# Optimization experiments

Hardware: AMD Instinct MI355X
Metric: run time of the kernel (lower is better)

Reference implementation:

```python
import jax, jax.numpy as jnp
import numpy as np

# dims
B, C, H, W = 32, 512, 32, 32
E, A, NC, DC, R, K = 256, 32, 8, 32, 24, 3
PW = NC * DC  # 256


def _ln(x, g, b, eps=1e-5):
    m = jnp.mean(x, axis=-1, keepdims=True)
    v = jnp.mean(jnp.square(x - m), axis=-1, keepdims=True)
    return (x - m) / jnp.sqrt(v + eps) * g + b


def setup_inputs() -> dict:
    key = jax.random.key(0)
    ks = jax.random.split(key, 12)
    s = 0.05
    f32 = jnp.float32
    return {
        "x": jax.random.normal(ks[0], (B, C, H, W), f32),
        "geo_state": jax.random.normal(ks[1], (B, PW), f32) * s,
        "W_svd": jax.random.normal(ks[2], (R, PW), f32) * s,
        "b_svd": jnp.zeros((PW,), f32),
        "g_svd": jnp.ones((PW,), f32),
        "beta_svd": jnp.zeros((PW,), f32),
        "W_emb": jax.random.normal(ks[3], (C, E), f32) * s,
        "g_emb": jnp.ones((E,), f32),
        "beta_emb": jnp.zeros((E,), f32),
        "anchors": jax.random.normal(ks[4], (A, E), f32),
        "Wc1": jax.random.normal(ks[5], (NC, A, 2 * DC), f32) * s,
        "bc1": jnp.zeros((NC, 2 * DC), f32),
        "Wc2": jax.random.normal(ks[6], (NC, 2 * DC, DC), f32) * s,
        "bc2": jnp.zeros((NC, DC), f32),
        "g_c": jnp.ones((NC, DC), f32),
        "beta_c": jnp.zeros((NC, DC), f32),
        "W_mod": jax.random.normal(ks[7], (3 * PW, C), f32) * s,
        "b_mod": jnp.zeros((C,), f32),
        "geo_gate": jnp.full((PW,), -3.0, f32),
        "W_geo": jax.random.normal(ks[8], (PW, PW), f32) * s,
        "b_geo": jnp.zeros((PW,), f32),
        "g_geo": jnp.ones((PW,), f32),
        "beta_geo": jnp.zeros((PW,), f32),
    }


def reference(x, geo_state, W_svd, b_svd, g_svd, beta_svd, W_emb, g_emb,
              beta_emb, anchors, Wc1, bc1, Wc2, bc2, g_c, beta_c, W_mod,
              b_mod, geo_gate, W_geo, b_geo, g_geo, beta_geo):
    Bx, Cx, Hx, Wx = x.shape
    HWx = Hx * Wx
    # --- SVD observer: top-R singular values via channel Gram eigvals ---
    X = x.reshape(Bx, Cx, HWx)
    Gm = jnp.einsum('bcn,bdn->bcd', X, X) / HWx           # (B, C, C)
    ev = jnp.linalg.eigvalsh(Gm)                           # ascending
    S = jnp.sqrt(jnp.clip(ev[:, ::-1][:, :R], 0.0))        # (B, R)
    svd_raw = jnp.log1p(S)
    svd_ctx = jax.nn.gelu(_ln(svd_raw @ W_svd + b_svd, g_svd, beta_svd),
                          approximate=False)               # (B, PW)
    # --- embedding: 1x1 conv + global avg pool (commute) + LN + L2 norm ---
    emb = jnp.einsum('bchw,ce->be', x, W_emb) / HWx        # (B, E)
    emb = _ln(emb, g_emb, beta_emb)
    emb = emb / jnp.maximum(jnp.linalg.norm(emb, axis=-1, keepdims=True), 1e-12)
    # --- anchor cosine geometry (anchors detached) ---
    an = anchors / jnp.maximum(jnp.linalg.norm(anchors, axis=-1, keepdims=True), 1e-12)
    an = jax.lax.stop_gradient(an)
    cos = emb @ an.T                                       # (B, A)
    tri = 1.0 - cos
    # --- cm_gate: softmax over n_neighbors nearest anchors ---
    topv, topi = jax.lax.top_k(cos, K)
    wgt = jax.nn.softmax(topv, axis=-1)                    # (B, K)
    oneh = jax.nn.one_hot(topi, A, dtype=x.dtype)          # (B, K, A)
    gate_values = jnp.einsum('bk,bka->ba', wgt, oneh)      # (B, A)
    tri_gated = tri * gate_values
    # --- grouped compartment MLPs (the Python loop, batched) ---
    h = jax.nn.gelu(jnp.einsum('ba,cad->bcd', tri_gated, Wc1) + bc1,
                    approximate=False)                     # (B, NC, 2*DC)
    pc = jnp.einsum('bcd,cde->bce', h, Wc2) + bc2          # (B, NC, DC)
    pc = _ln(pc, g_c, beta_c)
    pw = pc.reshape(Bx, PW)
    # --- channel modulation ---
    mod_in = jnp.concatenate([pw, svd_ctx, geo_state], axis=-1)
    cw = jax.nn.sigmoid(mod_in @ W_mod + b_mod)            # (B, C)
    x_out = x * cw[:, :, None, None]
    # --- gated residual geo-state update ---
    g = jax.nn.sigmoid(geo_gate)
    geo_out = geo_state + g * _ln(pw @ W_geo + b_geo, g_geo, beta_geo)
    return (x_out, geo_out)
```

## Files before the change

kernel.cpp:

```cpp
#include <hip/hip_runtime.h>
#include <hip/hip_bf16.h>

typedef unsigned short u16;
typedef unsigned int u32;
typedef __attribute__((ext_vector_type(8))) short short8;
typedef __attribute__((ext_vector_type(4))) float f32x4;

#define NB 32
#define NC_ 512
#define HW 1024
#define NE 256
#define NA 32
#define NR 24
#define PW_ 256
#define MLAN 128
#define NV 56

__device__ inline float b2f(u16 u) { return __uint_as_float(((u32)u) << 16); }
__device__ inline u16 f2b(float f) {
    u32 x = __float_as_uint(f);
    u32 r = x + 0x7FFFu + ((x >> 16) & 1u);
    return (u16)(r >> 16);
}
__device__ inline float gelu_exact(float x) {
    return 0.5f * x * (1.0f + erff(x * 0.70710678118654752f));
}
__device__ inline float sigmoidf_(float x) { return 1.0f / (1.0f + expf(-x)); }

template <int NW>
__device__ inline float block_reduce_sum(float x, volatile float* red) {
#pragma unroll
    for (int m = 32; m >= 1; m >>= 1) x += __shfl_xor(x, m);
    const int lane = threadIdx.x & 63, wid = threadIdx.x >> 6;
    __syncthreads();
    if (lane == 0) red[wid] = x;
    __syncthreads();
    float s = 0.f;
#pragma unroll
    for (int i = 0; i < NW; i++) s += red[i];
    return s;
}

__global__ __launch_bounds__(256) void gram_kernel(const float* __restrict__ x,
                                                   u16* __restrict__ Gp) {
    __shared__ __align__(16) u16 Ai[128][72];
    __shared__ __align__(16) u16 Bj[128][72];
    const int b = blockIdx.y;
    const int i0 = (blockIdx.x >> 2) * 128;
    const int j0 = (blockIdx.x & 3) * 128;
    const int t = threadIdx.x;
    const int lane = t & 63, wid = t >> 6;
    const int wm = (wid >> 1) * 64, wn = (wid & 1) * 64;
    f32x4 acc[4][4] = {};
    const float* xb = x + (size_t)b * NC_ * HW;

    for (int kc = 0; kc < HW; kc += 64) {
#pragma unroll
        for (int i = 0; i < 8; i++) {
            int idx = t + 256 * i;
            int r = idx >> 4, c4 = (idx & 15) * 4;
            float4 qa = *(const float4*)(xb + (size_t)(i0 + r) * HW + kc + c4);
            float4 qb = *(const float4*)(xb + (size_t)(j0 + r) * HW + kc + c4);
            Ai[r][c4 + 0] = f2b(qa.x); Ai[r][c4 + 1] = f2b(qa.y);
            Ai[r][c4 + 2] = f2b(qa.z); Ai[r][c4 + 3] = f2b(qa.w);
            Bj[r][c4 + 0] = f2b(qb.x); Bj[r][c4 + 1] = f2b(qb.y);
            Bj[r][c4 + 2] = f2b(qb.z); Bj[r][c4 + 3] = f2b(qb.w);
        }
        __syncthreads();
#pragma unroll
        for (int ks = 0; ks < 64; ks += 32) {
            const int kk = ks + (lane >> 4) * 8;
            short8 af[4], bf[4];
#pragma unroll
            for (int m = 0; m < 4; m++) af[m] = *(const short8*)&Ai[wm + m * 16 + (lane & 15)][kk];
#pragma unroll
            for (int n = 0; n < 4; n++) bf[n] = *(const short8*)&Bj[wn + n * 16 + (lane & 15)][kk];
#pragma unroll
            for (int m = 0; m < 4; m++)
#pragma unroll
                for (int n = 0; n < 4; n++)
                    acc[m][n] = __builtin_amdgcn_mfma_f32_16x16x32_bf16(af[m], bf[n], acc[m][n], 0, 0, 0);
        }
        __syncthreads();
    }
    const float scale = 1.0f / 1024.0f;
    u16* Gb = Gp + (size_t)b * NC_ * NC_;
#pragma unroll
    for (int m = 0; m < 4; m++) {
#pragma unroll
        for (int n = 0; n < 4; n++) {
            int row = i0 + wm + m * 16 + (lane >> 4) * 4;
            int col = j0 + wn + n * 16 + (lane & 15);
#pragma unroll
            for (int r = 0; r < 4; r++)
                Gb[(size_t)(row + r) * NC_ + col] = f2b(acc[m][n][r] * scale);
        }
    }
}

__global__ __launch_bounds__(256) void colsum_kernel(const float* __restrict__ x,
                                                     float* __restrict__ cs) {
    const int row = blockIdx.x * 4 + (threadIdx.x >> 6);
    const int lane = threadIdx.x & 63;
    const float* p = x + (size_t)row * HW;
    float s = 0.f;
    for (int i = lane; i < HW; i += 64) s += p[i];
#pragma unroll
    for (int m = 32; m >= 1; m >>= 1) s += __shfl_xor(s, m);
    if (lane == 0) cs[row] = s;
}

__global__ __launch_bounds__(1024, 4) void lanczos_kernel(const u16* __restrict__ Gp,
                                                          float* __restrict__ V,
                                                          float* __restrict__ svd_raw) {
    __shared__ __align__(16) float Vl[NV][512];
    __shared__ __align__(16) float v[512], w[512];
    __shared__ float v2[528];
    __shared__ float wpart[16][8][68];
    __shared__ float sub2[2][512];
    __shared__ float red[16], red2[16];
    __shared__ float al[MLAN], be[MLAN + 1], cc[MLAN];
    const int b = blockIdx.x;
    const int t = threadIdx.x;
    const int lane = t & 63, wid = t >> 6;
    const int el = t & 511, half = t >> 9;
    const int e8 = el & 7, l8 = el >> 3;
    const u16* Gb = Gp + (size_t)b * NC_ * NC_;
    const u16* gp = Gb + (size_t)(wid * 32) * NC_ + lane * 8;
    float* Vb = V + (size_t)b * MLAN * 512;

    u32 h = (u32)el * 2654435761u ^ ((u32)b * 0x9E3779B9u);
    h ^= h >> 16; h *= 0x85EBCA6Bu; h ^= h >> 13; h *= 0xC2B2AE35u; h ^= h >> 16;
    float vt = (float)(h & 0xFFFFFFu) * (1.0f / 16777216.0f) - 0.5f;
    float nrm = block_reduce_sum<16>(half == 0 ? vt * vt : 0.f, red);
    vt *= rsqrtf(nrm);
    if (half == 0) {
        v[el] = vt;
        v2[e8 * 66 + l8] = vt;
        Vl[0][el] = vt;
    }
    float vprev = 0.f, beta = 0.f;
    __syncthreads();

    for (int j = 0; j < MLAN; j++) {
        float a0 = 0.f, a1 = 0.f, a2 = 0.f, a3 = 0.f;
        float a4 = 0.f, a5 = 0.f, a6 = 0.f, a7 = 0.f;
        const float* vk = v + wid * 32;
#pragma unroll 16
        for (int kk = 0; kk < 32; kk++) {
            short8 g = *(const short8*)(gp + (size_t)kk * NC_);
            float vv = vk[kk];
            a0 += b2f((u16)g[0]) * vv;
            a1 += b2f((u16)g[1]) * vv;
            a2 += b2f((u16)g[2]) * vv;
            a3 += b2f((u16)g[3]) * vv;
            a4 += b2f((u16)g[4]) * vv;
            a5 += b2f((u16)g[5]) * vv;
            a6 += b2f((u16)g[6]) * vv;
            a7 += b2f((u16)g[7]) * vv;
        }
        wpart[wid][0][lane] = a0; wpart[wid][1][lane] = a1;
        wpart[wid][2][lane] = a2; wpart[wid][3][lane] = a3;
        wpart[wid][4][lane] = a4; wpart[wid][5][lane] = a5;
        wpart[wid][6][lane] = a6; wpart[wid][7][lane] = a7;
        float ap = a0 * v2[lane] + a1 * v2[66 + lane]
                 + a2 * v2[132 + lane] + a3 * v2[198 + lane]
                 + a4 * v2[264 + lane] + a5 * v2[330 + lane]
                 + a6 * v2[396 + lane] + a7 * v2[462 + lane];
#pragma unroll
        for (int m = 32; m >= 1; m >>= 1) ap += __shfl_xor(ap, m);
        if (lane == 0) red[wid] = ap;
        __syncthreads();

        float acc = 0.f;
#pragma unroll
        for (int p = 0; p < 16; p++) acc += wpart[p][e8][l8];
        float alpha = 0.f;
#pragma unroll
        for (int i = 0; i < 16; i++) alpha += red[i];
        float wt = acc - alpha * vt - beta * vprev;
        if (half == 0) w[el] = wt;
        float pz = wt * wt;
#pragma unroll
        for (int m = 32; m >= 1; m >>= 1) pz += __shfl_xor(pz, m);
        if (lane == 0 && wid < 8) red2[wid] = pz;
        __syncthreads();
        float nb0 = 0.f;
#pragma unroll
        for (int i = 0; i < 8; i++) nb0 += red2[i];
        const float gscale = nb0 + alpha * alpha + beta * beta;

        float nb = 0.f;
        for (int pass = 0;; pass++) {
            const float4 wv0 = *(const float4*)&w[lane * 4];
            const float4 wv1 = *(const float4*)&w[256 + lane * 4];
            for (int i = wid; i <= j; i += 16) {
                float4 x0, x1;
                if (i < NV) {
                    x0 = *(const float4*)&Vl[i][lane * 4];
                    x1 = *(const float4*)&Vl[i][256 + lane * 4];
                } else {
                    const float* Vi = Vb + (size_t)i * 512;
                    x0 = *(const float4*)(Vi + lane * 4);
                    x1 = *(const float4*)(Vi + 256 + lane * 4);
                }
                float p = x0.x * wv0.x + x0.y * wv0.y + x0.z * wv0.z + x0.w * wv0.w
                        + x1.x * wv1.x + x1.y * wv1.y + x1.z * wv1.z + x1.w * wv1.w;
#pragma unroll
                for (int m = 32; m >= 1; m >>= 1) p += __shfl_xor(p, m);
                if (lane == 0) cc[i] = p;
            }
            __syncthreads();
            const int n = j + 1, ns = n >> 1;
            const int ib = half ? ns : 0, ie = half ? n : ns;
            float sub = 0.f;
            int i = ib;
            const int iLe = (ie < NV) ? ie : NV;
            for (; i + 4 <= iLe; i += 4)
                sub += cc[i + 0] * Vl[i + 0][el] + cc[i + 1] * Vl[i + 1][el]
                     + cc[i + 2] * Vl[i + 2][el] + cc[i + 3] * Vl[i + 3][el];
            for (; i < iLe; i++) sub += cc[i] * Vl[i][el];
            if (i < ib) i = ib;
            for (; i + 4 <= ie; i += 4)
                sub += cc[i + 0] * Vb[(size_t)(i + 0) * 512 + el]
                     + cc[i + 1] * Vb[(size_t)(i + 1) * 512 + el]
                     + cc[i + 2] * Vb[(size_t)(i + 2) * 512 + el]
                     + cc[i + 3] * Vb[(size_t)(i + 3) * 512 + el];
            for (; i < ie; i++) sub += cc[i] * Vb[(size_t)i * 512 + el];
            sub2[half][el] = sub;
            __syncthreads();
            wt = wt - sub2[0][el] - sub2[1][el];
            if (half == 0) w[el] = wt;
            float pn = wt * wt;
#pragma unroll
            for (int m = 32; m >= 1; m >>= 1) pn += __shfl_xor(pn, m);
            if (lane == 0 && wid < 8) red[wid] = pn;
            __syncthreads();
            nb = 0.f;
#pragma unroll
            for (int q = 0; q < 8; q++) nb += red[q];
            if (pass == 1 || (nb > 0.5f * nb0 && nb0 > 1e-8f * gscale)) break;
            nb0 = nb;
        }
        float betn = sqrtf(nb);
        bool ok = (betn > 1e-20f) && (betn == betn) && !isinf(betn);
        if (t == 0) { al[j] = alpha; be[j + 1] = ok ? betn : 0.f; }
        float inv = ok ? 1.0f / betn : 0.f;
        vprev = vt;
        vt = ok ? wt * inv : 0.f;
        if (half == 0) {
            v[el] = vt;
            v2[e8 * 66 + l8] = vt;
            if (j + 1 < NV) Vl[j + 1][el] = vt;
            else if (j + 1 < MLAN) Vb[(size_t)(j + 1) * 512 + el] = vt;
        }
        beta = ok ? betn : 0.f;
        __syncthreads();
    }

    if (t < NR) {
        float lo = 1e30f, hi = -1e30f;
        for (int i = 0; i < MLAN; i++) {
            float bl = (i > 0) ? fabsf(be[i]) : 0.f;
            float br = (i + 1 < MLAN) ? fabsf(be[i + 1]) : 0.f;
            lo = fminf(lo, al[i] - bl - br);
            hi = fmaxf(hi, al[i] + bl + br);
        }
        const int i0 = MLAN - 1 - t;
        for (int it = 0; it < 30; it++) {
            float mid = 0.5f * (lo + hi);
            int cnt = 0;
            float d = 1.0f;
            for (int i = 0; i < MLAN; i++) {
                float bb2 = (i > 0) ? be[i] * be[i] : 0.f;
                float dp = d;
                if (fabsf(dp) < 1e-30f) dp = (dp < 0.f) ? -1e-30f : 1e-30f;
                d = (al[i] - mid) - bb2 / dp;
                cnt += (d < 0.f);
            }
            if (cnt > i0) hi = mid; else lo = mid;
        }
        float ev = fmaxf(0.5f * (lo + hi), 0.f);
        float val = log1pf(sqrtf(ev));
        if (!(val == val) || isinf(val)) val = 1.0f;
        svd_raw[b * NR + t] = val;
    }
}

__global__ __launch_bounds__(256) void embgate_kernel(
    const float* __restrict__ cs, const float* __restrict__ W_emb,
    const float* __restrict__ g_emb, const float* __restrict__ beta_emb,
    const float* __restrict__ anchors, float* __restrict__ tg_out) {
    const int b = blockIdx.x, t = threadIdx.x;
    __shared__ float csl[512], embv[256], cosv[32], tgs[32];
    __shared__ float red[4];

    for (int i = t; i < 512; i += 256) csl[i] = cs[b * 512 + i];
    __syncthreads();

    float e = 0.f;
    for (int c = 0; c < 512; c++) e += csl[c] * W_emb[c * NE + t];
    e *= (1.0f / 1024.0f);
    float mean = block_reduce_sum<4>(e, red) * (1.0f / 256.0f);
    float dv = e - mean;
    float var = block_reduce_sum<4>(dv * dv, red) * (1.0f / 256.0f);
    e = dv * rsqrtf(var + 1e-5f) * g_emb[t] + beta_emb[t];
    float nn = block_reduce_sum<4>(e * e, red);
    e = e / fmaxf(sqrtf(nn), 1e-12f);
    embv[t] = e;
    __syncthreads();

    if (t < 32) {
        float p = 0.f, na = 0.f;
        for (int q = 0; q < 256; q++) {
            float av = anchors[t * NE + q];
            p += embv[q] * av;
            na += av * av;
        }
        cosv[t] = p / fmaxf(sqrtf(na), 1e-12f);
    }
    __syncthreads();

    if (t == 0) {
        int i1 = 0, i2 = 0, i3 = 0;
        float v1 = -1e30f, v2 = -1e30f, v3 = -1e30f;
        for (int a = 0; a < 32; a++) {
            float cv = cosv[a];
            if (cv > v1) { v3 = v2; i3 = i2; v2 = v1; i2 = i1; v1 = cv; i1 = a; }
            else if (cv > v2) { v3 = v2; i3 = i2; v2 = cv; i2 = a; }
            else if (cv > v3) { v3 = cv; i3 = a; }
        }
        float e2 = expf(v2 - v1), e3 = expf(v3 - v1);
        float ss = 1.0f + e2 + e3;
        for (int a = 0; a < 32; a++) tgs[a] = 0.f;
        tgs[i1] = (1.0f - v1) * 1.0f / ss;
        tgs[i2] = (1.0f - v2) * e2 / ss;
        tgs[i3] = (1.0f - v3) * e3 / ss;
    }
    __syncthreads();
    if (t < 32) tg_out[b * 32 + t] = tgs[t];
}

__global__ __launch_bounds__(256) void mlp_kernel(
    const float* __restrict__ tg, const float* __restrict__ Wc1,
    const float* __restrict__ bc1, const float* __restrict__ Wc2,
    const float* __restrict__ bc2, const float* __restrict__ g_c,
    const float* __restrict__ beta_c, float* __restrict__ pw_out) {
    const int b = blockIdx.x, t = threadIdx.x;
    __shared__ float tgl[32], hbuf[512], pcb[256];

    if (t < 32) tgl[t] = tg[b * 32 + t];
    __syncthreads();

    for (int o = t; o < 512; o += 256) {
        int c = o >> 6, d = o & 63;
        float s = bc1[c * 64 + d];
        for (int a = 0; a < 32; a++) s += tgl[a] * Wc1[(c * 32 + a) * 64 + d];
        hbuf[o] = gelu_exact(s);
    }
    __syncthreads();

    const int c = t >> 5, e = t & 31;
    float s = bc2[c * 32 + e];
    for (int d = 0; d < 64; d++) s += hbuf[c * 64 + d] * Wc2[(c * 64 + d) * 32 + e];
    pcb[t] = s;
    __syncthreads();

    float mean = 0.f;
    for (int k = 0; k < 32; k++) mean += pcb[c * 32 + k];
    mean *= (1.0f / 32.0f);
    float var = 0.f;
    for (int k = 0; k < 32; k++) { float dd = pcb[c * 32 + k] - mean; var += dd * dd; }
    var *= (1.0f / 32.0f);
    pw_out[b * PW_ + t] = (s - mean) * rsqrtf(var + 1e-5f) * g_c[c * 32 + e] + beta_c[c * 32 + e];
}

__global__ __launch_bounds__(256) void ctx_kernel(
    const float* __restrict__ svd_raw, const float* __restrict__ W_svd,
    const float* __restrict__ b_svd, const float* __restrict__ g_svd,
    const float* __restrict__ beta_svd, float* __restrict__ ctx_out) {
    const int b = blockIdx.x, t = threadIdx.x;
    __shared__ float rawv[NR];
    __shared__ float red[4];
    if (t < NR) rawv[t] = svd_raw[b * NR + t];
    __syncthreads();
    float sv = b_svd[t];
    for (int r = 0; r < NR; r++) sv += rawv[r] * W_svd[r * PW_ + t];
    float mean = block_reduce_sum<4>(sv, red) * (1.0f / 256.0f);
    float dv = sv - mean;
    float var = block_reduce_sum<4>(dv * dv, red) * (1.0f / 256.0f);
    ctx_out[b * PW_ + t] = gelu_exact(dv * rsqrtf(var + 1e-5f) * g_svd[t] + beta_svd[t]);
}

__global__ __launch_bounds__(256) void cwgeo_kernel(
    const float* __restrict__ pw, const float* __restrict__ ctx,
    const float* __restrict__ geo_state, const float* __restrict__ W_mod,
    const float* __restrict__ b_mod, const float* __restrict__ geo_gate,
    const float* __restrict__ W_geo, const float* __restrict__ b_geo,
    const float* __restrict__ g_geo, const float* __restrict__ beta_geo,
    float* __restrict__ cw, float* __restrict__ out_geo) {
    const int b = blockIdx.x, t = threadIdx.x;
    __shared__ float mi[768];
    __shared__ float red[4];
    mi[t] = pw[b * PW_ + t];
    mi[256 + t] = ctx[b * PW_ + t];
    float geo = geo_state[b * PW_ + t];
    mi[512 + t] = geo;
    __syncthreads();

    float gg = b_geo[t];
    for (int q = 0; q < PW_; q++) gg += mi[q] * W_geo[q * PW_ + t];
    float gmean = block_reduce_sum<4>(gg, red) * (1.0f / 256.0f);
    float gdv = gg - gmean;
    float gvar = block_reduce_sum<4>(gdv * gdv, red) * (1.0f / 256.0f);
    float lnv = gdv * rsqrtf(gvar + 1e-5f) * g_geo[t] + beta_geo[t];
    out_geo[b * PW_ + t] = geo + sigmoidf_(geo_gate[t]) * lnv;

    for (int c = t; c < 512; c += 256) {
        float s = b_mod[c];
        for (int k = 0; k < 768; k++) s += mi[k] * W_mod[k * NC_ + c];
        cw[b * NC_ + c] = sigmoidf_(s);
    }
}

__global__ __launch_bounds__(256) void modulate_kernel(const float* __restrict__ x,
                                                       const float* __restrict__ cw,
                                                       float* __restrict__ out) {
    const int i4 = blockIdx.x * 256 + threadIdx.x;
    const float4* xp = (const float4*)x;
    float4 q = xp[i4];
    const float wv = cw[i4 >> 8];
    float4 o;
    o.x = q.x * wv; o.y = q.y * wv; o.z = q.z * wv; o.w = q.w * wv;
    ((float4*)out)[i4] = o;
}

extern "C" void kernel_launch(void* const* d_in, const int* in_sizes, int n_in,
                              void* d_out, int out_size, void* d_ws, size_t ws_size,
                              hipStream_t stream) {
    const float* x = (const float*)d_in[0];
    const float* geo_state = (const float*)d_in[1];
    const float* W_svd = (const float*)d_in[2];
    const float* b_svd = (const float*)d_in[3];
    const float* g_svd = (const float*)d_in[4];
    const float* beta_svd = (const float*)d_in[5];
    const float* W_emb = (const float*)d_in[6];
    const float* g_emb = (const float*)d_in[7];
    const float* beta_emb = (const float*)d_in[8];
    const float* anchors = (const float*)d_in[9];
    const float* Wc1 = (const float*)d_in[10];
    const float* bc1 = (const float*)d_in[11];
    const float* Wc2 = (const float*)d_in[12];
    const float* bc2 = (const float*)d_in[13];
    const float* g_c = (const float*)d_in[14];
    const float* beta_c = (const float*)d_in[15];
    const float* W_mod = (const float*)d_in[16];
    const float* b_mod = (const float*)d_in[17];
    const float* geo_gate = (const float*)d_in[18];
    const float* W_geo = (const float*)d_in[19];
    const float* b_geo = (const float*)d_in[20];
    const float* g_geo = (const float*)d_in[21];
    const float* beta_geo = (const float*)d_in[22];

    char* ob = (char*)d_out;
    u16* G = (u16*)(ob);
    float* V = (float*)(ob + 16777216);
    float* cs = (float*)(ob + 25165824);
    float* svdraw = (float*)(ob + 25231360);
    float* tg = (float*)(ob + 25234432);
    float* pw = (float*)(ob + 25238528);
    float* ctxb = (float*)(ob + 25271296);
    float* cw = (float*)d_ws;

    float* outx = (float*)d_out;
    float* outg = outx + 16777216;

    gram_kernel<<<dim3(16, 32), dim3(256), 0, stream>>>(x, G);
    colsum_kernel<<<dim3(4096), dim3(256), 0, stream>>>(x, cs);
    lanczos_kernel<<<dim3(32), dim3(1024), 0, stream>>>(G, V, svdraw);
    embgate_kernel<<<dim3(32), dim3(256), 0, stream>>>(cs, W_emb, g_emb, beta_emb, anchors, tg);
    mlp_kernel<<<dim3(32), dim3(256), 0, stream>>>(tg, Wc1, bc1, Wc2, bc2, g_c, beta_c, pw);
    ctx_kernel<<<dim3(32), dim3(256), 0, stream>>>(svdraw, W_svd, b_svd, g_svd, beta_svd, ctxb);
    cwgeo_kernel<<<dim3(32), dim3(256), 0, stream>>>(pw, ctxb, geo_state, W_mod, b_mod,
                                                     geo_gate, W_geo, b_geo, g_geo, beta_geo,
                                                     cw, outg);
    modulate_kernel<<<dim3(16384), dim3(256), 0, stream>>>(x, cw, outx);
}
```

Measured before the change: 1.847 ms.

## Store unnormalized Lanczos vectors, fuse reorthogonalization subtraction, cache Gram rows in registers

The Lanczos loop now keeps unnormalized residual vectors and applies the 1/beta scaling lazily through per-vector scale factors (sc2_, invc). That removes the separate normalize-and-store step and the barrier at the end of each iteration. Reorthogonalization projection and subtraction are fused: each wave accumulates its p*V contributions in registers and writes them to a shared scratch buffer. This replaces the cc array and the second half-split subtraction pass with its extra barrier. The first 12 rows of each wave's bf16 Gram slice are preloaded into registers, which raises register pressure at 1024 threads per block and may change numerical stability slightly.

After: 2.011 ms. 1.09x slower.

```diff
diff --git a/kernel.cpp b/kernel.cpp
--- a/kernel.cpp
+++ b/kernel.cpp
@@ -15,6 +15,7 @@
 #define PW_ 256
 #define MLAN 128
 #define NV 56
+#define NCACHE 12
 
 __device__ inline float b2f(u16 u) { return __uint_as_float(((u32)u) << 16); }
 __device__ inline u16 f2b(float f) {
@@ -114,12 +115,11 @@
                                                           float* __restrict__ V,
                                                           float* __restrict__ svd_raw) {
     __shared__ __align__(16) float Vl[NV][512];
-    __shared__ __align__(16) float v[512], w[512];
+    __shared__ __align__(16) float w[512];
     __shared__ float v2[528];
-    __shared__ float wpart[16][8][68];
-    __shared__ float sub2[2][512];
-    __shared__ float red[16], red2[16];
-    __shared__ float al[MLAN], be[MLAN + 1], cc[MLAN];
+    __shared__ __align__(16) float scr[16][544];
+    __shared__ float red[16], red2[8], red3[8];
+    __shared__ float al[MLAN], be[MLAN + 1], sc2_[MLAN + 1];
     const int b = blockIdx.x;
     const int t = threadIdx.x;
     const int lane = t & 63, wid = t >> 6;
@@ -129,25 +129,35 @@
     const u16* gp = Gb + (size_t)(wid * 32) * NC_ + lane * 8;
     float* Vb = V + (size_t)b * MLAN * 512;
 
+    u32 gc[NCACHE * 4];
+#pragma unroll
+    for (int kk = 0; kk < NCACHE; kk++) {
+        short8 g = *(const short8*)(gp + (size_t)kk * NC_);
+        const u32* gu = (const u32*)&g;
+        gc[kk * 4 + 0] = gu[0]; gc[kk * 4 + 1] = gu[1];
+        gc[kk * 4 + 2] = gu[2]; gc[kk * 4 + 3] = gu[3];
+    }
+
     u32 h = (u32)el * 2654435761u ^ ((u32)b * 0x9E3779B9u);
     h ^= h >> 16; h *= 0x85EBCA6Bu; h ^= h >> 13; h *= 0xC2B2AE35u; h ^= h >> 16;
-    float vt = (float)(h & 0xFFFFFFu) * (1.0f / 16777216.0f) - 0.5f;
-    float nrm = block_reduce_sum<16>(half == 0 ? vt * vt : 0.f, red);
-    vt *= rsqrtf(nrm);
+    float vt0 = (float)(h & 0xFFFFFFu) * (1.0f / 16777216.0f) - 0.5f;
+    float nrm = block_reduce_sum<16>(half == 0 ? vt0 * vt0 : 0.f, red);
+    vt0 *= rsqrtf(nrm);
     if (half == 0) {
-        v[el] = vt;
-        v2[e8 * 66 + l8] = vt;
-        Vl[0][el] = vt;
-    }
-    float vprev = 0.f, beta = 0.f;
+        w[el] = vt0;
+        v2[e8 * 66 + l8] = vt0;
+        Vl[0][el] = vt0;
+    }
+    if (t == 0) sc2_[0] = 1.0f;
+    float rw = vt0, invc = 1.0f, rwp = 0.f, invp = 0.f, beta = 0.f;
     __syncthreads();
 
     for (int j = 0; j < MLAN; j++) {
         float a0 = 0.f, a1 = 0.f, a2 = 0.f, a3 = 0.f;
         float a4 = 0.f, a5 = 0.f, a6 = 0.f, a7 = 0.f;
-        const float* vk = v + wid * 32;
-#pragma unroll 16
-        for (int kk = 0; kk < 32; kk++) {
+        const float* vk = w + wid * 32;
+#pragma unroll 5
+        for (int kk = NCACHE; kk < 32; kk++) {
             short8 g = *(const short8*)(gp + (size_t)kk * NC_);
             float vv = vk[kk];
             a0 += b2f((u16)g[0]) * vv;
@@ -159,10 +169,24 @@
             a6 += b2f((u16)g[6]) * vv;
             a7 += b2f((u16)g[7]) * vv;
         }
-        wpart[wid][0][lane] = a0; wpart[wid][1][lane] = a1;
-        wpart[wid][2][lane] = a2; wpart[wid][3][lane] = a3;
-        wpart[wid][4][lane] = a4; wpart[wid][5][lane] = a5;
-        wpart[wid][6][lane] = a6; wpart[wid][7][lane] = a7;
+#pragma unroll
+        for (int kk = 0; kk < NCACHE; kk++) {
+            float vv = vk[kk];
+            u32 u0 = gc[kk * 4 + 0], u1 = gc[kk * 4 + 1];
+            u32 u2 = gc[kk * 4 + 2], u3 = gc[kk * 4 + 3];
+            a0 += __uint_as_float(u0 << 16) * vv;
+            a1 += __uint_as_float(u0 & 0xFFFF0000u) * vv;
+            a2 += __uint_as_float(u1 << 16) * vv;
+            a3 += __uint_as_float(u1 & 0xFFFF0000u) * vv;
+            a4 += __uint_as_float(u2 << 16) * vv;
+            a5 += __uint_as_float(u2 & 0xFFFF0000u) * vv;
+            a6 += __uint_as_float(u3 << 16) * vv;
+            a7 += __uint_as_float(u3 & 0xFFFF0000u) * vv;
+        }
+        scr[wid][0 * 68 + lane] = a0; scr[wid][1 * 68 + lane] = a1;
+        scr[wid][2 * 68 + lane] = a2; scr[wid][3 * 68 + lane] = a3;
+        scr[wid][4 * 68 + lane] = a4; scr[wid][5 * 68 + lane] = a5;
+        scr[wid][6 * 68 + lane] = a6; scr[wid][7 * 68 + lane] = a7;
         float ap = a0 * v2[lane] + a1 * v2[66 + lane]
                  + a2 * v2[132 + lane] + a3 * v2[198 + lane]
                  + a4 * v2[264 + lane] + a5 * v2[330 + lane]
@@ -172,13 +196,14 @@
         if (lane == 0) red[wid] = ap;
         __syncthreads();
 
-        float acc = 0.f;
-#pragma unroll
-        for (int p = 0; p < 16; p++) acc += wpart[p][e8][l8];
-        float alpha = 0.f;
-#pragma unroll
-        for (int i = 0; i < 16; i++) alpha += red[i];
-        float wt = acc - alpha * vt - beta * vprev;
+        float accp = 0.f;
+#pragma unroll
+        for (int p = 0; p < 16; p++) accp += scr[p][e8 * 68 + l8];
+        float rawa = 0.f;
+#pragma unroll
+        for (int i = 0; i < 16; i++) rawa += red[i];
+        const float alpha = rawa * invc * invc;
+        float wt = accp * invc - alpha * (rw * invc) - beta * (rwp * invp);
         if (half == 0) w[el] = wt;
         float pz = wt * wt;
 #pragma unroll
@@ -194,6 +219,8 @@
         for (int pass = 0;; pass++) {
             const float4 wv0 = *(const float4*)&w[lane * 4];
             const float4 wv1 = *(const float4*)&w[256 + lane * 4];
+            float s0 = 0.f, s1 = 0.f, s2 = 0.f, s3 = 0.f;
+            float s4 = 0.f, s5 = 0.f, s6 = 0.f, s7 = 0.f;
             for (int i = wid; i <= j; i += 16) {
                 float4 x0, x1;
                 if (i < NV) {
@@ -208,54 +235,45 @@
                         + x1.x * wv1.x + x1.y * wv1.y + x1.z * wv1.z + x1.w * wv1.w;
 #pragma unroll
                 for (int m = 32; m >= 1; m >>= 1) p += __shfl_xor(p, m);
-                if (lane == 0) cc[i] = p;
+                const float ps = p * sc2_[i];
+                s0 += ps * x0.x; s1 += ps * x0.y; s2 += ps * x0.z; s3 += ps * x0.w;
+                s4 += ps * x1.x; s5 += ps * x1.y; s6 += ps * x1.z; s7 += ps * x1.w;
             }
+            *(f32x4*)&scr[wid][lane * 4] = (f32x4){s0, s1, s2, s3};
+            *(f32x4*)&scr[wid][256 + lane * 4] = (f32x4){s4, s5, s6, s7};
             __syncthreads();
-            const int n = j + 1, ns = n >> 1;
-            const int ib = half ? ns : 0, ie = half ? n : ns;
             float sub = 0.f;
-            int i = ib;
-            const int iLe = (ie < NV) ? ie : NV;
-            for (; i + 4 <= iLe; i += 4)
-                sub += cc[i + 0] * Vl[i + 0][el] + cc[i + 1] * Vl[i + 1][el]
-                     + cc[i + 2] * Vl[i + 2][el] + cc[i + 3] * Vl[i + 3][el];
-            for (; i < iLe; i++) sub += cc[i] * Vl[i][el];
-            if (i < ib) i = ib;
-            for (; i + 4 <= ie; i += 4)
-                sub += cc[i + 0] * Vb[(size_t)(i + 0) * 512 + el]
-                     + cc[i + 1] * Vb[(size_t)(i + 1) * 512 + el]
-                     + cc[i + 2] * Vb[(size_t)(i + 2) * 512 + el]
-                     + cc[i + 3] * Vb[(size_t)(i + 3) * 512 + el];
-            for (; i < ie; i++) sub += cc[i] * Vb[(size_t)i * 512 + el];
-            sub2[half][el] = sub;
-            __syncthreads();
-            wt = wt - sub2[0][el] - sub2[1][el];
-            if (half == 0) w[el] = wt;
+#pragma unroll
+            for (int p16 = 0; p16 < 16; p16++) sub += scr[p16][el];
+            wt = wt - sub;
+            if (half == 0) {
+                w[el] = wt;
+                v2[e8 * 66 + l8] = wt;
+                if (j + 1 < NV) Vl[j + 1][el] = wt;
+                else if (j + 1 < MLAN) Vb[(size_t)(j + 1) * 512 + el] = wt;
+            }
             float pn = wt * wt;
 #pragma unroll
             for (int m = 32; m >= 1; m >>= 1) pn += __shfl_xor(pn, m);
-            if (lane == 0 && wid < 8) red[wid] = pn;
+            if (lane == 0 && wid < 8) red3[wid] = pn;
             __syncthreads();
             nb = 0.f;
 #pragma unroll
-            for (int q = 0; q < 8; q++) nb += red[q];
+            for (int q = 0; q < 8; q++) nb += red3[q];
             if (pass == 1 || (nb > 0.5f * nb0 && nb0 > 1e-8f * gscale)) break;
             nb0 = nb;
         }
         float betn = sqrtf(nb);
         bool ok = (betn > 1e-20f) && (betn == betn) && !isinf(betn);
-        if (t == 0) { al[j] = alpha; be[j + 1] = ok ? betn : 0.f; }
-        float inv = ok ? 1.0f / betn : 0.f;
-        vprev = vt;
-        vt = ok ? wt * inv : 0.f;
-        if (half == 0) {
-            v[el] = vt;
-            v2[e8 * 66 + l8] = vt;
-            if (j + 1 < NV) Vl[j + 1][el] = vt;
-            else if (j + 1 < MLAN) Vb[(size_t)(j + 1) * 512 + el] = vt;
+        if (t == 0) {
+            al[j] = alpha;
+            be[j + 1] = ok ? betn : 0.f;
+            sc2_[j + 1] = ok ? 1.0f / nb : 0.f;
         }
         beta = ok ? betn : 0.f;
-        __syncthreads();
+        rwp = rw; invp = invc;
+        rw = wt;
+        invc = ok ? 1.0f / betn : 0.f;
     }
 
     if (t < NR) {
```
